# Kernel optimization log

Measured on AMD Instinct MI355X. Metric: run time of the kernel, lower is better.

## Reference

```python
import jax, jax.numpy as jnp
import numpy as np

E = 1024
H = 16
T = 2048
B = 2
HD = E // H


def setup_inputs() -> dict:
    key = jax.random.key(0)
    ks = jax.random.split(key, 12)
    s = 1.0 / np.sqrt(E)
    return {
        "x": jax.random.normal(ks[0], (T, B, E), dtype=jnp.float32),
        "padding_mask": jax.random.randint(ks[1], (B, T), 0, 2) > 0,
        "attn_bias": jax.random.normal(ks[2], (B * H, T, T), dtype=jnp.float32) * 0.02,
        "Wq": jax.random.normal(ks[3], (E, E), dtype=jnp.float32) * s,
        "bq": jnp.zeros((E,), dtype=jnp.float32),
        "Wk": jax.random.normal(ks[4], (E, E), dtype=jnp.float32) * s,
        "bk": jnp.zeros((E,), dtype=jnp.float32),
        "Wv": jax.random.normal(ks[5], (E, E), dtype=jnp.float32) * s,
        "bv": jnp.zeros((E,), dtype=jnp.float32),
        "Wo": jax.random.normal(ks[6], (E, E), dtype=jnp.float32) * s,
        "bo": jnp.zeros((E,), dtype=jnp.float32),
    }


def reference(x, padding_mask, attn_bias, Wq, bq, Wk, bk, Wv, bv, Wo, bo):
    tgt_len, bsz, embed_dim = x.shape
    head_dim = embed_dim // H
    scaling = head_dim ** -0.5
    # projections (torch Linear: y = x @ W.T + b)
    q = (x @ Wq.T + bq) * scaling  # [T,B,E]
    k = x @ Wk.T + bk
    v = x @ Wv.T + bv
    q = q.reshape(tgt_len, bsz, H, head_dim)
    k = k.reshape(tgt_len, bsz, H, head_dim)
    v = v.reshape(tgt_len, bsz, H, head_dim)
    # QK^T -> [B,H,T,S]
    attn_weights = jnp.einsum("tbhd,sbhd->bhts", q, k)
    # masked_fill with -1e-16 (as in original source)
    mask = padding_mask[:, None, None, :]  # [B,1,1,S]
    attn_weights = jnp.where(mask, jnp.float32(-1e-16), attn_weights)
    attn_weights = attn_weights + attn_bias.reshape(bsz, H, tgt_len, tgt_len)
    attn_probs = jax.nn.softmax(attn_weights, axis=-1)
    # AV -> back to [T,B,E]
    attn = jnp.einsum("bhts,sbhd->tbhd", attn_probs, v).reshape(tgt_len, bsz, embed_dim)
    return attn @ Wo.T + bo
```

## Files before the change

kernel.cpp:

```cpp
#include <hip/hip_runtime.h>

#define E_DIM 1024
#define H_DIM 16
#define T_DIM 2048
#define B_DIM 2
#define HD_DIM 64
#define NROWS (T_DIM*B_DIM)

typedef unsigned short u16;
typedef unsigned long long u64;
typedef __attribute__((ext_vector_type(8))) short bf16x8;
typedef __attribute__((ext_vector_type(4))) float f32x4;

__device__ __forceinline__ u16 f2bf(float f){
  unsigned int u = __float_as_uint(f);
  u = u + 0x7fffu + ((u>>16)&1u);
  return (u16)(u>>16);
}

__device__ __forceinline__ void gl_lds16(const u16* g, u16* l){
  __builtin_amdgcn_global_load_lds(
      (const __attribute__((address_space(1))) void*)g,
      (__attribute__((address_space(3))) void*)l, 16, 0, 0);
}

#define DPP_F(v, op, ctrl) \
  v = op(v, __int_as_float(__builtin_amdgcn_mov_dpp(__float_as_int(v), ctrl, 0xf, 0xf, true)))
__device__ __forceinline__ float fadd_(float a, float b){ return a + b; }

__global__ __launch_bounds__(256) void convert_f32_bf16(
    const float* __restrict__ src, u16* __restrict__ dst, int n4)
{
  int i = blockIdx.x*256 + threadIdx.x;
  if (i < n4){
    float4 f = ((const float4*)src)[i];
    u64 pack =  (u64)f2bf(f.x)
             | ((u64)f2bf(f.y) << 16)
             | ((u64)f2bf(f.z) << 32)
             | ((u64)f2bf(f.w) << 48);
    ((u64*)dst)[i] = pack;
  }
}

__global__ __launch_bounds__(256) void gemm_qkv(
    const u16* __restrict__ xb, const u16* __restrict__ wb,
    const float* __restrict__ bq, const float* __restrict__ bk,
    const float* __restrict__ bv,
    u16* __restrict__ qb, u16* __restrict__ kb, u16* __restrict__ vtb)
{
  __shared__ u16 sA[128*32];
  __shared__ u16 sB[128*32];
  int tid = threadIdx.x;
  int w = tid >> 6, lane = tid & 63;
  int qd = lane >> 4, l15 = lane & 15;
  int wr = w >> 1, wc = w & 1;
  int row0 = blockIdx.y*128;
  int col0 = blockIdx.x*128;

  int srow = tid >> 2;
  int scol = (tid & 3) * 8;
  const u16* ga0 = xb + (size_t)(row0 + srow)*E_DIM + scol;
  const u16* ga1 = xb + (size_t)(row0 + 64 + srow)*E_DIM + scol;
  const u16* gb0 = wb + (size_t)(col0 + srow)*E_DIM + scol;
  const u16* gb1 = wb + (size_t)(col0 + 64 + srow)*E_DIM + scol;
  u16* lA0 = sA + tid*8;
  u16* lA1 = sA + 2048 + tid*8;
  u16* lB0 = sB + tid*8;
  u16* lB1 = sB + 2048 + tid*8;

  f32x4 z = {0.f,0.f,0.f,0.f};
  f32x4 acc[4][4];
  for (int i=0;i<4;i++) for (int j=0;j<4;j++) acc[i][j] = z;

  const u16* pa = sA + (wr*64 + l15)*32 + qd*8;
  const u16* pb = sB + (wc*64 + l15)*32 + qd*8;

  for (int kk = 0; kk < E_DIM; kk += 32){
    gl_lds16(ga0 + kk, lA0);
    gl_lds16(ga1 + kk, lA1);
    gl_lds16(gb0 + kk, lB0);
    gl_lds16(gb1 + kk, lB1);
    __syncthreads();
    bf16x8 a[4], bfr[4];
#pragma unroll
    for (int i=0;i<4;i++){
      a[i]   = *(const bf16x8*)(pa + i*512);
      bfr[i] = *(const bf16x8*)(pb + i*512);
    }
#pragma unroll
    for (int i=0;i<4;i++)
#pragma unroll
      for (int j=0;j<4;j++)
        acc[i][j] = __builtin_amdgcn_mfma_f32_16x16x32_bf16(a[i], bfr[j], acc[i][j], 0,0,0);
    __syncthreads();
  }

#pragma unroll
  for (int j=0;j<4;j++){
    int n = col0 + wc*64 + j*16 + l15;
    int p = n >> 10;
    int e = n & 1023;
    int hh = e >> 6, d = e & 63;
    float bias = (p==0) ? bq[e] : (p==1) ? bk[e] : bv[e];
#pragma unroll
    for (int i=0;i<4;i++){
#pragma unroll
      for (int r=0;r<4;r++){
        int row = row0 + wr*64 + i*16 + qd*4 + r;
        int t = row >> 1, b = row & 1;
        float val = acc[i][j][r] + bias;
        if (p == 0){
          val *= 0.125f;
          qb[((size_t)((b*H_DIM+hh)*T_DIM + t))*HD_DIM + d] = f2bf(val);
        } else if (p == 1){
          kb[((size_t)((b*H_DIM+hh)*T_DIM + t))*HD_DIM + d] = f2bf(val);
        } else {
          vtb[((size_t)((b*H_DIM+hh)*HD_DIM + d))*T_DIM + t] = f2bf(val);
        }
      }
    }
  }
}

__global__ __launch_bounds__(256) void attn_kernel(
    const u16* __restrict__ qb, const u16* __restrict__ kb,
    const u16* __restrict__ vtb, const float* __restrict__ bias,
    const void* __restrict__ pmask, u16* __restrict__ attnb)
{
  __shared__ u16 p_lds[4][16][32];
  __shared__ int s_bytemode;
  int tid = threadIdx.x;
  if (tid == 0) s_bytemode = 0;
  __syncthreads();
  {
    const unsigned char* pb_ = (const unsigned char*)pmask;
    unsigned char c = pb_[tid*4+1] | pb_[tid*4+2] | pb_[tid*4+3];
    if (c) s_bytemode = 1;
  }
  __syncthreads();
  int bytemode = s_bytemode;

  int w = tid >> 6, lane = tid & 63;
  int qd = lane >> 4, l15 = lane & 15;
  int bh = blockIdx.y;
  int b = bh >> 4;
  int hh = bh & 15;
  int trow0 = blockIdx.x*64 + w*16;

  const u16* qh = qb + (size_t)bh * T_DIM * HD_DIM;
  const u16* kh = kb + (size_t)bh * T_DIM * HD_DIM;
  const u16* vh = vtb + (size_t)bh * HD_DIM * T_DIM;
  const float* biash = bias + (size_t)bh * T_DIM * T_DIM;
  const int* pmi = (const int*)pmask;
  const unsigned char* pmb = (const unsigned char*)pmask;

  int tq = trow0 + l15;
  bf16x8 aq0 = *(const bf16x8*)(qh + (size_t)tq*HD_DIM + qd*8);
  bf16x8 aq1 = *(const bf16x8*)(qh + (size_t)tq*HD_DIM + 32 + qd*8);

  f32x4 z = {0.f,0.f,0.f,0.f};
  f32x4 o[4]; for (int i=0;i<4;i++) o[i] = z;
  float m_r[4] = {-1e30f,-1e30f,-1e30f,-1e30f};
  float l_r[4] = {0.f,0.f,0.f,0.f};

  int trq = trow0 + qd*4;

  bf16x8 k00 = *(const bf16x8*)(kh + (size_t)(l15)*HD_DIM + qd*8);
  bf16x8 k01 = *(const bf16x8*)(kh + (size_t)(l15)*HD_DIM + 32 + qd*8);
  bf16x8 k10 = *(const bf16x8*)(kh + (size_t)(16+l15)*HD_DIM + qd*8);
  bf16x8 k11 = *(const bf16x8*)(kh + (size_t)(16+l15)*HD_DIM + 32 + qd*8);
  float pb0[4], pb1[4];
#pragma unroll
  for (int r=0;r<4;r++){
    pb0[r] = biash[(size_t)(trq+r)*T_DIM + l15];
    pb1[r] = biash[(size_t)(trq+r)*T_DIM + 16 + l15];
  }

  for (int s0 = 0; s0 < T_DIM; s0 += 32){
    int sn = (s0 + 32 < T_DIM) ? (s0 + 32) : 0;
    bf16x8 nk00 = *(const bf16x8*)(kh + (size_t)(sn+l15)*HD_DIM + qd*8);
    bf16x8 nk01 = *(const bf16x8*)(kh + (size_t)(sn+l15)*HD_DIM + 32 + qd*8);
    bf16x8 nk10 = *(const bf16x8*)(kh + (size_t)(sn+16+l15)*HD_DIM + qd*8);
    bf16x8 nk11 = *(const bf16x8*)(kh + (size_t)(sn+16+l15)*HD_DIM + 32 + qd*8);
    float nb0[4], nb1[4];
#pragma unroll
    for (int r=0;r<4;r++){
      nb0[r] = biash[(size_t)(trq+r)*T_DIM + sn + l15];
      nb1[r] = biash[(size_t)(trq+r)*T_DIM + sn + 16 + l15];
    }

    int sc0 = s0 + l15, sc1 = s0 + 16 + l15;
    bool msk0 = bytemode ? (pmb[b*T_DIM + sc0] != 0) : (pmi[b*T_DIM + sc0] != 0);
    bool msk1 = bytemode ? (pmb[b*T_DIM + sc1] != 0) : (pmi[b*T_DIM + sc1] != 0);

    f32x4 sA = __builtin_amdgcn_mfma_f32_16x16x32_bf16(aq1, k01, z, 0,0,0);
    sA       = __builtin_amdgcn_mfma_f32_16x16x32_bf16(aq0, k00, sA, 0,0,0);
    f32x4 sB = __builtin_amdgcn_mfma_f32_16x16x32_bf16(aq1, k11, z, 0,0,0);
    sB       = __builtin_amdgcn_mfma_f32_16x16x32_bf16(aq0, k10, sB, 0,0,0);

#pragma unroll
    for (int r=0;r<4;r++){
      float v0 = (msk0 ? -1e-16f : sA[r]) + pb0[r];
      float v1 = (msk1 ? -1e-16f : sB[r]) + pb1[r];
      float tm = fmaxf(v0, v1);
      DPP_F(tm, fmaxf, 0xB1);
      DPP_F(tm, fmaxf, 0x4E);
      DPP_F(tm, fmaxf, 0x141);
      DPP_F(tm, fmaxf, 0x140);
      float mn = fmaxf(m_r[r], tm);
      float alpha = __expf(m_r[r] - mn);
      float p0 = __expf(v0 - mn);
      float p1 = __expf(v1 - mn);
      float rs = p0 + p1;
      DPP_F(rs, fadd_, 0xB1);
      DPP_F(rs, fadd_, 0x4E);
      DPP_F(rs, fadd_, 0x141);
      DPP_F(rs, fadd_, 0x140);
      l_r[r] = l_r[r]*alpha + rs;
      m_r[r] = mn;
      o[0][r] *= alpha; o[1][r] *= alpha; o[2][r] *= alpha; o[3][r] *= alpha;
      p_lds[w][qd*4+r][l15]      = f2bf(p0);
      p_lds[w][qd*4+r][16 + l15] = f2bf(p1);
    }
    __asm__ __volatile__("s_waitcnt lgkmcnt(0)" ::: "memory");

    bf16x8 ap = *(const bf16x8*)(&p_lds[w][l15][qd*8]);
#pragma unroll
    for (int dt=0; dt<4; dt++){
      bf16x8 bv = *(const bf16x8*)(vh + (size_t)(dt*16 + l15)*T_DIM + s0 + qd*8);
      o[dt] = __builtin_amdgcn_mfma_f32_16x16x32_bf16(ap, bv, o[dt], 0,0,0);
    }

    k00 = nk00; k01 = nk01; k10 = nk10; k11 = nk11;
#pragma unroll
    for (int r=0;r<4;r++){ pb0[r] = nb0[r]; pb1[r] = nb1[r]; }
  }

#pragma unroll
  for (int dt=0; dt<4; dt++){
#pragma unroll
    for (int r=0;r<4;r++){
      int t = trow0 + qd*4 + r;
      float val = o[dt][r] / l_r[r];
      attnb[(size_t)(t*B_DIM + b)*E_DIM + hh*HD_DIM + dt*16 + l15] = f2bf(val);
    }
  }
}

__global__ __launch_bounds__(256) void gemm_out(
    const u16* __restrict__ ab, const u16* __restrict__ wob,
    const float* __restrict__ bo, float* __restrict__ out)
{
  __shared__ u16 sA[128*32];
  __shared__ u16 sB[128*32];
  int tid = threadIdx.x;
  int w = tid >> 6, lane = tid & 63;
  int qd = lane >> 4, l15 = lane & 15;
  int wr = w >> 1, wc = w & 1;
  int row0 = blockIdx.y*128;
  int col0 = blockIdx.x*128;

  int srow = tid >> 2;
  int scol = (tid & 3) * 8;
  const u16* ga0 = ab + (size_t)(row0 + srow)*E_DIM + scol;
  const u16* ga1 = ab + (size_t)(row0 + 64 + srow)*E_DIM + scol;
  const u16* gb0 = wob + (size_t)(col0 + srow)*E_DIM + scol;
  const u16* gb1 = wob + (size_t)(col0 + 64 + srow)*E_DIM + scol;
  u16* lA0 = sA + tid*8;
  u16* lA1 = sA + 2048 + tid*8;
  u16* lB0 = sB + tid*8;
  u16* lB1 = sB + 2048 + tid*8;

  f32x4 z = {0.f,0.f,0.f,0.f};
  f32x4 acc[4][4];
  for (int i=0;i<4;i++) for (int j=0;j<4;j++) acc[i][j] = z;

  const u16* pa = sA + (wr*64 + l15)*32 + qd*8;
  const u16* pb = sB + (wc*64 + l15)*32 + qd*8;

  for (int kk = 0; kk < E_DIM; kk += 32){
    gl_lds16(ga0 + kk, lA0);
    gl_lds16(ga1 + kk, lA1);
    gl_lds16(gb0 + kk, lB0);
    gl_lds16(gb1 + kk, lB1);
    __syncthreads();
    bf16x8 a[4], bfr[4];
#pragma unroll
    for (int i=0;i<4;i++){
      a[i]   = *(const bf16x8*)(pa + i*512);
      bfr[i] = *(const bf16x8*)(pb + i*512);
    }
#pragma unroll
    for (int i=0;i<4;i++)
#pragma unroll
      for (int j=0;j<4;j++)
        acc[i][j] = __builtin_amdgcn_mfma_f32_16x16x32_bf16(a[i], bfr[j], acc[i][j], 0,0,0);
    __syncthreads();
  }

#pragma unroll
  for (int j=0;j<4;j++){
    int n = col0 + wc*64 + j*16 + l15;
    float bias = bo[n];
#pragma unroll
    for (int i=0;i<4;i++){
#pragma unroll
      for (int r=0;r<4;r++){
        int row = row0 + wr*64 + i*16 + qd*4 + r;
        out[(size_t)row*E_DIM + n] = acc[i][j][r] + bias;
      }
    }
  }
}

extern "C" void kernel_launch(void* const* d_in, const int* in_sizes, int n_in,
                              void* d_out, int out_size, void* d_ws, size_t ws_size,
                              hipStream_t stream) {
  const float* x    = (const float*)d_in[0];
  const void*  pm   = d_in[1];
  const float* abias= (const float*)d_in[2];
  const float* Wq   = (const float*)d_in[3];
  const float* bq   = (const float*)d_in[4];
  const float* Wk   = (const float*)d_in[5];
  const float* bk   = (const float*)d_in[6];
  const float* Wv   = (const float*)d_in[7];
  const float* bv   = (const float*)d_in[8];
  const float* Wo   = (const float*)d_in[9];
  const float* bo   = (const float*)d_in[10];
  float* out = (float*)d_out;

  char* ws = (char*)d_ws;
  u16* xb    = (u16*)(ws);
  u16* wqkvb = (u16*)(ws + (8u<<20));
  u16* wob   = (u16*)(ws + (14u<<20));
  u16* qb    = (u16*)(ws + (16u<<20));
  u16* kb    = (u16*)(ws + (24u<<20));
  u16* vtb   = (u16*)(ws + (32u<<20));
  u16* attnb = (u16*)(ws + (40u<<20));

  {
    int n4x = (T_DIM*B_DIM*E_DIM)/4;
    convert_f32_bf16<<<dim3(n4x/256), 256, 0, stream>>>(x, xb, n4x);
    int n4w = (E_DIM*E_DIM)/4;
    convert_f32_bf16<<<dim3(n4w/256), 256, 0, stream>>>(Wq, wqkvb,                 n4w);
    convert_f32_bf16<<<dim3(n4w/256), 256, 0, stream>>>(Wk, wqkvb + (1u<<20),      n4w);
    convert_f32_bf16<<<dim3(n4w/256), 256, 0, stream>>>(Wv, wqkvb + (2u<<20),      n4w);
    convert_f32_bf16<<<dim3(n4w/256), 256, 0, stream>>>(Wo, wob,                   n4w);
  }

  gemm_qkv<<<dim3(3*E_DIM/128, NROWS/128), 256, 0, stream>>>(
      xb, wqkvb, bq, bk, bv, qb, kb, vtb);

  attn_kernel<<<dim3(T_DIM/64, B_DIM*H_DIM), 256, 0, stream>>>(
      qb, kb, vtb, abias, pm, attnb);

  gemm_out<<<dim3(E_DIM/128, NROWS/128), 256, 0, stream>>>(
      attnb, wob, bo, out);
}
```

Baseline: 959.4 us.

## Split attention key range across wave pairs, swizzle GEMM blocks, narrow output tiles

The attention kernel now runs 512 threads per block. Two groups of four waves each process half of the key sequence for the same query rows, and their partial softmax states are merged through shared memory at the end. This doubles the number of resident waves working on the bandwidth-heavy bias stream. Both GEMMs gain a block-index swizzle for better L2 locality, and the output GEMM drops to 128x64 tiles to launch more blocks. The costs are a larger LDS footprint, an extra block barrier, and register pressure under launch_bounds(512,8).

```diff
diff --git a/kernel.cpp b/kernel.cpp
--- a/kernel.cpp
+++ b/kernel.cpp
@@ -54,8 +54,13 @@
   int w = tid >> 6, lane = tid & 63;
   int qd = lane >> 4, l15 = lane & 15;
   int wr = w >> 1, wc = w & 1;
-  int row0 = blockIdx.y*128;
-  int col0 = blockIdx.x*128;
+
+  unsigned bid = blockIdx.y * 24u + blockIdx.x;
+  unsigned swz = (bid & 7u) * 96u + (bid >> 3);
+  int bx = (int)(swz % 24u);
+  int by = (int)(swz / 24u);
+  int row0 = by*128;
+  int col0 = bx*128;
 
   int srow = tid >> 2;
   int scol = (tid & 3) * 8;
@@ -122,12 +127,14 @@
   }
 }
 
-__global__ __launch_bounds__(256) void attn_kernel(
+__global__ __launch_bounds__(512, 8) void attn_kernel(
     const u16* __restrict__ qb, const u16* __restrict__ kb,
     const u16* __restrict__ vtb, const float* __restrict__ bias,
     const void* __restrict__ pmask, u16* __restrict__ attnb)
 {
-  __shared__ u16 p_lds[4][16][32];
+  __shared__ u16 p_lds[8][16][32];
+  __shared__ float c_o[4][64][16];
+  __shared__ float c_ml[4][64][8];
   __shared__ int s_bytemode;
   int tid = threadIdx.x;
   if (tid == 0) s_bytemode = 0;
@@ -140,12 +147,15 @@
   __syncthreads();
   int bytemode = s_bytemode;
 
-  int w = tid >> 6, lane = tid & 63;
+  int wid = tid >> 6, lane = tid & 63;
+  int pair = wid & 3, shalf = wid >> 2;
   int qd = lane >> 4, l15 = lane & 15;
   int bh = blockIdx.y;
   int b = bh >> 4;
   int hh = bh & 15;
-  int trow0 = blockIdx.x*64 + w*16;
+  int trow0 = blockIdx.x*64 + pair*16;
+  int sbeg = shalf * (T_DIM/2);
+  int send = sbeg + (T_DIM/2);
 
   const u16* qh = qb + (size_t)bh * T_DIM * HD_DIM;
   const u16* kh = kb + (size_t)bh * T_DIM * HD_DIM;
@@ -165,19 +175,19 @@
 
   int trq = trow0 + qd*4;
 
-  bf16x8 k00 = *(const bf16x8*)(kh + (size_t)(l15)*HD_DIM + qd*8);
-  bf16x8 k01 = *(const bf16x8*)(kh + (size_t)(l15)*HD_DIM + 32 + qd*8);
-  bf16x8 k10 = *(const bf16x8*)(kh + (size_t)(16+l15)*HD_DIM + qd*8);
-  bf16x8 k11 = *(const bf16x8*)(kh + (size_t)(16+l15)*HD_DIM + 32 + qd*8);
+  bf16x8 k00 = *(const bf16x8*)(kh + (size_t)(sbeg+l15)*HD_DIM + qd*8);
+  bf16x8 k01 = *(const bf16x8*)(kh + (size_t)(sbeg+l15)*HD_DIM + 32 + qd*8);
+  bf16x8 k10 = *(const bf16x8*)(kh + (size_t)(sbeg+16+l15)*HD_DIM + qd*8);
+  bf16x8 k11 = *(const bf16x8*)(kh + (size_t)(sbeg+16+l15)*HD_DIM + 32 + qd*8);
   float pb0[4], pb1[4];
 #pragma unroll
   for (int r=0;r<4;r++){
-    pb0[r] = biash[(size_t)(trq+r)*T_DIM + l15];
-    pb1[r] = biash[(size_t)(trq+r)*T_DIM + 16 + l15];
-  }
-
-  for (int s0 = 0; s0 < T_DIM; s0 += 32){
-    int sn = (s0 + 32 < T_DIM) ? (s0 + 32) : 0;
+    pb0[r] = biash[(size_t)(trq+r)*T_DIM + sbeg + l15];
+    pb1[r] = biash[(size_t)(trq+r)*T_DIM + sbeg + 16 + l15];
+  }
+
+  for (int s0 = sbeg; s0 < send; s0 += 32){
+    int sn = (s0 + 32 < send) ? (s0 + 32) : sbeg;
     bf16x8 nk00 = *(const bf16x8*)(kh + (size_t)(sn+l15)*HD_DIM + qd*8);
     bf16x8 nk01 = *(const bf16x8*)(kh + (size_t)(sn+l15)*HD_DIM + 32 + qd*8);
     bf16x8 nk10 = *(const bf16x8*)(kh + (size_t)(sn+16+l15)*HD_DIM + qd*8);
@@ -219,12 +229,12 @@
       l_r[r] = l_r[r]*alpha + rs;
       m_r[r] = mn;
       o[0][r] *= alpha; o[1][r] *= alpha; o[2][r] *= alpha; o[3][r] *= alpha;
-      p_lds[w][qd*4+r][l15]      = f2bf(p0);
-      p_lds[w][qd*4+r][16 + l15] = f2bf(p1);
+      p_lds[wid][qd*4+r][l15]      = f2bf(p0);
+      p_lds[wid][qd*4+r][16 + l15] = f2bf(p1);
     }
     __asm__ __volatile__("s_waitcnt lgkmcnt(0)" ::: "memory");
 
-    bf16x8 ap = *(const bf16x8*)(&p_lds[w][l15][qd*8]);
+    bf16x8 ap = *(const bf16x8*)(&p_lds[wid][l15][qd*8]);
 #pragma unroll
     for (int dt=0; dt<4; dt++){
       bf16x8 bv = *(const bf16x8*)(vh + (size_t)(dt*16 + l15)*T_DIM + s0 + qd*8);
@@ -236,13 +246,31 @@
     for (int r=0;r<4;r++){ pb0[r] = nb0[r]; pb1[r] = nb1[r]; }
   }
 
-#pragma unroll
-  for (int dt=0; dt<4; dt++){
+  if (shalf == 1){
 #pragma unroll
     for (int r=0;r<4;r++){
+      c_ml[pair][lane][r]   = m_r[r];
+      c_ml[pair][lane][4+r] = l_r[r];
+#pragma unroll
+      for (int dt=0;dt<4;dt++) c_o[pair][lane][dt*4+r] = o[dt][r];
+    }
+  }
+  __syncthreads();
+  if (shalf == 0){
+#pragma unroll
+    for (int r=0;r<4;r++){
+      float m2 = c_ml[pair][lane][r];
+      float l2 = c_ml[pair][lane][4+r];
+      float mn = fmaxf(m_r[r], m2);
+      float a1 = __expf(m_r[r] - mn);
+      float a2 = __expf(m2 - mn);
+      float lt = l_r[r]*a1 + l2*a2;
       int t = trow0 + qd*4 + r;
-      float val = o[dt][r] / l_r[r];
-      attnb[(size_t)(t*B_DIM + b)*E_DIM + hh*HD_DIM + dt*16 + l15] = f2bf(val);
+#pragma unroll
+      for (int dt=0;dt<4;dt++){
+        float val = (o[dt][r]*a1 + c_o[pair][lane][dt*4+r]*a2) / lt;
+        attnb[(size_t)(t*B_DIM + b)*E_DIM + hh*HD_DIM + dt*16 + l15] = f2bf(val);
+      }
     }
   }
 }
@@ -252,55 +280,56 @@
     const float* __restrict__ bo, float* __restrict__ out)
 {
   __shared__ u16 sA[128*32];
-  __shared__ u16 sB[128*32];
+  __shared__ u16 sB[64*32];
   int tid = threadIdx.x;
   int w = tid >> 6, lane = tid & 63;
   int qd = lane >> 4, l15 = lane & 15;
   int wr = w >> 1, wc = w & 1;
-  int row0 = blockIdx.y*128;
-  int col0 = blockIdx.x*128;
+
+  unsigned bid = blockIdx.y * 16u + blockIdx.x;
+  unsigned swz = (bid & 7u) * 64u + (bid >> 3);
+  int bx = (int)(swz % 16u);
+  int by = (int)(swz / 16u);
+  int row0 = by*128;
+  int col0 = bx*64;
 
   int srow = tid >> 2;
   int scol = (tid & 3) * 8;
   const u16* ga0 = ab + (size_t)(row0 + srow)*E_DIM + scol;
   const u16* ga1 = ab + (size_t)(row0 + 64 + srow)*E_DIM + scol;
   const u16* gb0 = wob + (size_t)(col0 + srow)*E_DIM + scol;
-  const u16* gb1 = wob + (size_t)(col0 + 64 + srow)*E_DIM + scol;
   u16* lA0 = sA + tid*8;
   u16* lA1 = sA + 2048 + tid*8;
   u16* lB0 = sB + tid*8;
-  u16* lB1 = sB + 2048 + tid*8;
 
   f32x4 z = {0.f,0.f,0.f,0.f};
-  f32x4 acc[4][4];
-  for (int i=0;i<4;i++) for (int j=0;j<4;j++) acc[i][j] = z;
+  f32x4 acc[4][2];
+  for (int i=0;i<4;i++) for (int j=0;j<2;j++) acc[i][j] = z;
 
   const u16* pa = sA + (wr*64 + l15)*32 + qd*8;
-  const u16* pb = sB + (wc*64 + l15)*32 + qd*8;
+  const u16* pb = sB + (wc*32 + l15)*32 + qd*8;
 
   for (int kk = 0; kk < E_DIM; kk += 32){
     gl_lds16(ga0 + kk, lA0);
     gl_lds16(ga1 + kk, lA1);
     gl_lds16(gb0 + kk, lB0);
-    gl_lds16(gb1 + kk, lB1);
     __syncthreads();
-    bf16x8 a[4], bfr[4];
-#pragma unroll
-    for (int i=0;i<4;i++){
-      a[i]   = *(const bf16x8*)(pa + i*512);
-      bfr[i] = *(const bf16x8*)(pb + i*512);
-    }
+    bf16x8 a[4], bfr[2];
+#pragma unroll
+    for (int i=0;i<4;i++) a[i] = *(const bf16x8*)(pa + i*512);
+#pragma unroll
+    for (int j=0;j<2;j++) bfr[j] = *(const bf16x8*)(pb + j*512);
 #pragma unroll
     for (int i=0;i<4;i++)
 #pragma unroll
-      for (int j=0;j<4;j++)
+      for (int j=0;j<2;j++)
         acc[i][j] = __builtin_amdgcn_mfma_f32_16x16x32_bf16(a[i], bfr[j], acc[i][j], 0,0,0);
     __syncthreads();
   }
 
 #pragma unroll
-  for (int j=0;j<4;j++){
-    int n = col0 + wc*64 + j*16 + l15;
+  for (int j=0;j<2;j++){
+    int n = col0 + wc*32 + j*16 + l15;
     float bias = bo[n];
 #pragma unroll
     for (int i=0;i<4;i++){
@@ -351,9 +380,9 @@
   gemm_qkv<<<dim3(3*E_DIM/128, NROWS/128), 256, 0, stream>>>(
       xb, wqkvb, bq, bk, bv, qb, kb, vtb);
 
-  attn_kernel<<<dim3(T_DIM/64, B_DIM*H_DIM), 256, 0, stream>>>(
+  attn_kernel<<<dim3(T_DIM/64, B_DIM*H_DIM), 512, 0, stream>>>(
       qb, kb, vtb, abias, pm, attnb);
 
-  gemm_out<<<dim3(E_DIM/128, NROWS/128), 256, 0, stream>>>(
+  gemm_out<<<dim3(E_DIM/64, NROWS/128), 256, 0, stream>>>(
       attnb, wob, bo, out);
 }
```

Measured after the change: 1.992 ms. 108% more time.
